# Kernel optimization log

Measured on AMD Instinct MI355X. Metric: run time of the kernel, lower is better.

The kernel has to match this reference:

```python
import jax, jax.numpy as jnp
import numpy as np

TOP_K = 2
AUX_COEF = 1e-3

def setup_inputs() -> dict:
    key = jax.random.key(0)
    ks = jax.random.split(key, 5)
    B, S, H, I, E = 4, 2048, 1024, 2048, 8
    x = jax.random.normal(ks[0], (B, S, H), jnp.float32)
    gate_w = jax.random.normal(ks[1], (H, E), jnp.float32) * 0.02
    w_gate = jax.random.normal(ks[2], (E, H, I), jnp.float32) * 0.02
    w_up = jax.random.normal(ks[3], (E, H, I), jnp.float32) * 0.02
    w_down = jax.random.normal(ks[4], (E, I, H), jnp.float32) * 0.02
    return {"x": x, "gate_w": gate_w, "w_gate": w_gate, "w_up": w_up, "w_down": w_down}


def reference(x, gate_w, w_gate, w_up, w_down):
    B, S, H = x.shape
    E = gate_w.shape[1]
    xf = x.reshape(-1, H)              # [N, H]
    N = xf.shape[0]

    # Router: softmax in fp32 (matches F.softmax(..., dtype=torch.float32))
    logits = xf @ gate_w               # [N, E]
    rw = jax.nn.softmax(logits.astype(jnp.float32), axis=-1).astype(x.dtype)
    top_w, top_i = jax.lax.top_k(rw, TOP_K)            # [N, K]
    top_w = top_w / top_w.sum(axis=-1, keepdims=True)  # renormalize

    # Combine weights: comb[t, e] = sum_k top_w[t,k] * (top_i[t,k]==e)
    comb = jnp.zeros((N, E), x.dtype).at[jnp.arange(N)[:, None], top_i].add(top_w)

    # SwiGLU FFN computed densely per expert, masked/combined by router weights
    h_gate = jax.nn.silu(jnp.einsum('th,ehi->eti', xf, w_gate))   # [E, N, I]
    h_up = jnp.einsum('th,ehi->eti', xf, w_up)                    # [E, N, I]
    expert_out = jnp.einsum('eti,eih->eth', h_gate * h_up, w_down)  # [E, N, H]
    y = jnp.einsum('eth,te->th', expert_out, comb).reshape(B, S, H)

    # Load-balancing aux loss
    sel_w = jnp.take_along_axis(rw, top_i, axis=1)   # router weight of chosen experts [N, K]
    load = jnp.zeros((E,), rw.dtype).at[top_i.reshape(-1)].add(sel_w.reshape(-1))
    P_expert = load / N
    counts = jnp.zeros((E,), jnp.float32).at[top_i.reshape(-1)].add(1.0)
    P_token_expert = counts / (N * TOP_K)
    aux_loss = (P_expert * P_token_expert).sum() * E * AUX_COEF
    return y, aux_loss
```

## Files before the change

kernel.cpp:

```cpp
#include <hip/hip_runtime.h>

#define N_TOK 8192
#define H_DIM 1024
#define I_DIM 2048
#define N_EXP 8
#define TOPK  2
#define CAP   17408
#define MT_MAX 136

#define OFF_TOPK_I 0u
#define OFF_TOPK_W 65536u
#define OFF_COUNTS 131072u
#define OFF_LOAD   131104u
#define OFF_CURSOR 131136u
#define OFF_PO     131168u
#define OFF_TILE_E 131232u
#define OFF_BTOK   131840u
#define OFF_BW     201472u
#define CTRL_BYTES 271104u
#define OFF_TSLOT  271104u
#define OFF_WGT  1048576u
#define OFF_WUT  (OFF_WGT + 33554432u)
#define OFF_WDT  (OFF_WUT + 33554432u)
#define OFF_HB   (OFF_WDT + 33554432u)
#define OFF_XB   (OFF_HB + 71303168u)

typedef __attribute__((ext_vector_type(8))) short bf16x8;
typedef __attribute__((ext_vector_type(8))) unsigned short u16x8;
typedef __attribute__((ext_vector_type(4))) unsigned short u16x4;
typedef __attribute__((ext_vector_type(4))) float f32x4;

__device__ __forceinline__ unsigned short f2bf(float f) {
  union { float f; unsigned int u; } v; v.f = f;
  unsigned int r = (v.u + 0x7FFFu + ((v.u >> 16) & 1u)) >> 16;
  return (unsigned short)r;
}
__device__ __forceinline__ float bf2f(unsigned short u) {
  union { unsigned int u; float f; } v; v.u = ((unsigned int)u) << 16;
  return v.f;
}
__device__ __forceinline__ u16x8 pack8(float4 a, float4 b) {
  u16x8 r;
  r[0] = f2bf(a.x); r[1] = f2bf(a.y); r[2] = f2bf(a.z); r[3] = f2bf(a.w);
  r[4] = f2bf(b.x); r[5] = f2bf(b.y); r[6] = f2bf(b.z); r[7] = f2bf(b.w);
  return r;
}
__device__ __forceinline__ f32x4 mfma32(bf16x8 a, bf16x8 b, f32x4 c) {
  return __builtin_amdgcn_mfma_f32_16x16x32_bf16(a, b, c, 0, 0, 0);
}
__device__ __forceinline__ void gll16(const void* g, void* l) {
  __builtin_amdgcn_global_load_lds(
      (const __attribute__((address_space(1))) unsigned int*)g,
      (__attribute__((address_space(3))) unsigned int*)l, 16, 0, 0);
}

__global__ __launch_bounds__(256) void k_xcast(const float* __restrict__ x,
                                               unsigned short* __restrict__ xb)
{
  int idx = blockIdx.x * 256 + threadIdx.x;
  const float4* s = (const float4*)x + (size_t)idx * 2;
  float4 a = s[0], b = s[1];
  *(u16x8*)&xb[(size_t)idx * 8] = pack8(a, b);
}

__global__ __launch_bounds__(256) void k_transpose(
    const float* __restrict__ wg, const float* __restrict__ wu, const float* __restrict__ wd,
    unsigned short* __restrict__ wgT, unsigned short* __restrict__ wuT,
    unsigned short* __restrict__ wdT)
{
  __shared__ unsigned short lds[64][65];
  int bid = blockIdx.x;
  int m = bid / 4096; int rem = bid % 4096;
  const float* src; unsigned short* dst; int R, C;
  if (m == 0)      { src = wg; dst = wgT; R = 1024; C = 2048; }
  else if (m == 1) { src = wu; dst = wuT; R = 1024; C = 2048; }
  else             { src = wd; dst = wdT; R = 2048; C = 1024; }
  int e = rem / 512; int trem = rem % 512;
  int tcc = C / 64;
  int r0 = (trem / tcc) * 64, c0 = (trem % tcc) * 64;
  size_t ebase = (size_t)e * R * C;
  dst += ebase;
  int tid = threadIdx.x;
  int lr = tid >> 3;
  int lc = (tid & 7) * 8;
#pragma unroll
  for (int p = 0; p < 2; ++p) {
    int row = p * 32 + lr;
    size_t off = ebase + (size_t)(r0 + row) * C + c0 + lc;
    float4 q0 = *(const float4*)&src[off];
    float4 q1 = *(const float4*)&src[off + 4];
    unsigned short tmp[8]; *(u16x8*)tmp = pack8(q0, q1);
#pragma unroll
    for (int j = 0; j < 8; ++j) lds[row][lc + j] = tmp[j];
  }
  __syncthreads();
#pragma unroll
  for (int p = 0; p < 2; ++p) {
    int drow = p * 32 + lr;
    unsigned short tmp[8];
#pragma unroll
    for (int j = 0; j < 8; ++j) tmp[j] = lds[lc + j][drow];
    *(u16x8*)&dst[(size_t)(c0 + drow) * R + r0 + lc] = *(const u16x8*)tmp;
  }
}

__global__ __launch_bounds__(256) void k_router(
    const float* __restrict__ x, const float* __restrict__ gw,
    int* __restrict__ topk_i, float* __restrict__ topk_w)
{
  int wave = threadIdx.x >> 6, lane = threadIdx.x & 63;
  int t = blockIdx.x * 4 + wave;
  const float* xr = x + (size_t)t * H_DIM;
  float acc[8];
#pragma unroll
  for (int e = 0; e < 8; ++e) acc[e] = 0.f;
#pragma unroll
  for (int it = 0; it < H_DIM / 64; ++it) {
    int h = it * 64 + lane;
    float xv = xr[h];
    float4 g0 = *(const float4*)&gw[h * 8];
    float4 g1 = *(const float4*)&gw[h * 8 + 4];
    acc[0] += xv * g0.x; acc[1] += xv * g0.y; acc[2] += xv * g0.z; acc[3] += xv * g0.w;
    acc[4] += xv * g1.x; acc[5] += xv * g1.y; acc[6] += xv * g1.z; acc[7] += xv * g1.w;
  }
#pragma unroll
  for (int off = 32; off > 0; off >>= 1) {
#pragma unroll
    for (int e = 0; e < 8; ++e) acc[e] += __shfl_xor(acc[e], off);
  }
  if (lane == 0) {
    float m = acc[0];
#pragma unroll
    for (int e = 1; e < 8; ++e) m = fmaxf(m, acc[e]);
    float p[8], s = 0.f;
#pragma unroll
    for (int e = 0; e < 8; ++e) { p[e] = __expf(acc[e] - m); s += p[e]; }
    float inv = 1.f / s;
#pragma unroll
    for (int e = 0; e < 8; ++e) p[e] *= inv;
    int i1 = 0;
#pragma unroll
    for (int e = 1; e < 8; ++e) if (p[e] > p[i1]) i1 = e;
    int i2 = (i1 == 0) ? 1 : 0;
#pragma unroll
    for (int e = 0; e < 8; ++e) if (e != i1 && p[e] > p[i2]) i2 = e;
    topk_i[t * 2]     = i1; topk_i[t * 2 + 1] = i2;
    topk_w[t * 2]     = p[i1]; topk_w[t * 2 + 1] = p[i2];
  }
}

__global__ __launch_bounds__(256) void k_hist(
    const int* __restrict__ topk_i, const float* __restrict__ topk_w,
    int* __restrict__ counts, float* __restrict__ loadw)
{
  __shared__ int c[8]; __shared__ float l[8];
  int tid = threadIdx.x;
  if (tid < 8) { c[tid] = 0; l[tid] = 0.f; }
  __syncthreads();
  int base = blockIdx.x * 1024 + tid * 4;
#pragma unroll
  for (int j = 0; j < 4; ++j) {
    int e = topk_i[base + j];
    float w = topk_w[base + j];
    atomicAdd(&c[e], 1);
    atomicAdd(&l[e], w);
  }
  __syncthreads();
  if (tid < 8) { atomicAdd(&counts[tid], c[tid]); atomicAdd(&loadw[tid], l[tid]); }
}

__global__ __launch_bounds__(256) void k_offsets(
    const int* __restrict__ counts, const float* __restrict__ loadw,
    int* __restrict__ po, int* __restrict__ tile_e, float* __restrict__ out)
{
  __shared__ int spo[9];
  if (threadIdx.x == 0) {
    int a = 0;
    for (int e = 0; e < 8; ++e) { spo[e] = a; po[e] = a; a += (counts[e] + 127) & ~127; }
    spo[8] = a; po[8] = a;
    float s = 0.f;
    for (int e = 0; e < 8; ++e) s += loadw[e] * (float)counts[e];
    out[(size_t)N_TOK * H_DIM] =
        s * ((float)N_EXP * 1e-3f) / ((float)N_TOK * (float)N_TOK * (float)TOPK);
  }
  __syncthreads();
  int mt = threadIdx.x;
  if (mt < MT_MAX) {
    int te = -1, beg = mt * 128;
    if (beg < spo[8]) {
      for (int e = 0; e < 8; ++e) if (beg >= spo[e] && beg < spo[e + 1]) te = e;
    }
    tile_e[mt] = te;
  }
}

__global__ __launch_bounds__(256) void k_bucket(
    const int* __restrict__ topk_i, const float* __restrict__ topk_w,
    const int* __restrict__ po, int* __restrict__ cursor,
    int* __restrict__ btok, float* __restrict__ bw, int* __restrict__ tslot)
{
  __shared__ int c[8];
  __shared__ int basee[8];
  int tid = threadIdx.x;
  if (tid < 8) c[tid] = 0;
  __syncthreads();
  int base = blockIdx.x * 1024 + tid * 4;
  int e4[4], r4[4]; float w4[4];
#pragma unroll
  for (int j = 0; j < 4; ++j) {
    int idx = base + j;
    int e = topk_i[idx];
    e4[j] = e;
    r4[j] = atomicAdd(&c[e], 1);
    int t = idx >> 1;
    float p0 = topk_w[t * 2], p1 = topk_w[t * 2 + 1];
    w4[j] = topk_w[idx] / (p0 + p1);
  }
  __syncthreads();
  if (tid < 8) basee[tid] = po[tid] + atomicAdd(&cursor[tid], c[tid]);
  __syncthreads();
#pragma unroll
  for (int j = 0; j < 4; ++j) {
    int idx = base + j;
    int slot = basee[e4[j]] + r4[j];
    btok[slot] = idx >> 1;
    bw[slot] = w4[j];
    tslot[idx] = slot;
  }
}

__global__ __launch_bounds__(256, 2) void k_gemm1(
    const unsigned short* __restrict__ xb,
    const unsigned short* __restrict__ wgT, const unsigned short* __restrict__ wuT,
    const int* __restrict__ btok, const int* __restrict__ tile_e,
    unsigned short* __restrict__ hbuf)
{
  int mt = blockIdx.y, nt = blockIdx.x;
  int e = tile_e[mt];
  if (e < 0) return;
  __shared__ unsigned short As[128 * 32];
  __shared__ unsigned short Bg[128 * 32];
  __shared__ unsigned short Bu[128 * 32];
  int tid = threadIdx.x;
  int wave = tid >> 6, lane = tid & 63;
  int wm = wave >> 1, wn = wave & 1;
  int quad = lane >> 4, l16 = lane & 15;

  int srow = lane >> 2;
  int sko  = (lane & 3) * 8;
  int ar0 = wave * 16 + srow;
  int ar1 = 64 + wave * 16 + srow;
  int t0 = btok[mt * 128 + ar0];
  int t1 = btok[mt * 128 + ar1];
  const unsigned short* ga0 = xb + (size_t)t0 * H_DIM + sko;
  const unsigned short* ga1 = xb + (size_t)t1 * H_DIM + sko;
  const unsigned short* bgb = wgT + ((size_t)e * I_DIM + nt * 128) * H_DIM;
  const unsigned short* bub = wuT + ((size_t)e * I_DIM + nt * 128) * H_DIM;
  const unsigned short* gg0 = bgb + (size_t)ar0 * H_DIM + sko;
  const unsigned short* gg1 = bgb + (size_t)ar1 * H_DIM + sko;
  const unsigned short* gu0 = bub + (size_t)ar0 * H_DIM + sko;
  const unsigned short* gu1 = bub + (size_t)ar1 * H_DIM + sko;
  unsigned lb0 = (unsigned)(wave * 16) * 32;
  unsigned lb1 = (unsigned)(64 + wave * 16) * 32;

  f32x4 accG[4][4], accU[4][4];
  f32x4 z = {0.f, 0.f, 0.f, 0.f};
#pragma unroll
  for (int i = 0; i < 4; ++i)
#pragma unroll
    for (int j = 0; j < 4; ++j) { accG[i][j] = z; accU[i][j] = z; }

  for (int k0 = 0; k0 < H_DIM; k0 += 32) {
    gll16(ga0 + k0, &As[lb0]);
    gll16(ga1 + k0, &As[lb1]);
    gll16(gg0 + k0, &Bg[lb0]);
    gll16(gg1 + k0, &Bg[lb1]);
    gll16(gu0 + k0, &Bu[lb0]);
    gll16(gu1 + k0, &Bu[lb1]);
    __syncthreads();
    bf16x8 af[4];
#pragma unroll
    for (int i = 0; i < 4; ++i)
      af[i] = *(const bf16x8*)&As[(wm * 64 + i * 16 + l16) * 32 + quad * 8];
#pragma unroll
    for (int j = 0; j < 4; ++j) {
      bf16x8 vg = *(const bf16x8*)&Bg[(wn * 64 + j * 16 + l16) * 32 + quad * 8];
      bf16x8 vu = *(const bf16x8*)&Bu[(wn * 64 + j * 16 + l16) * 32 + quad * 8];
#pragma unroll
      for (int i = 0; i < 4; ++i) {
        accG[i][j] = mfma32(af[i], vg, accG[i][j]);
        accU[i][j] = mfma32(af[i], vu, accU[i][j]);
      }
    }
    __syncthreads();
  }
#pragma unroll
  for (int i = 0; i < 4; ++i) {
#pragma unroll
    for (int r = 0; r < 4; ++r) {
      int row = mt * 128 + wm * 64 + i * 16 + quad * 4 + r;
      size_t base = (size_t)row * I_DIM + nt * 128 + wn * 64 + l16;
#pragma unroll
      for (int j = 0; j < 4; ++j) {
        float g = accG[i][j][r], u = accU[i][j][r];
        float sg = g / (1.f + __expf(-g));
        hbuf[base + j * 16] = f2bf(sg * u);
      }
    }
  }
}

__global__ __launch_bounds__(256, 2) void k_gemm2(
    const unsigned short* __restrict__ hbuf, const unsigned short* __restrict__ wdT,
    const int* __restrict__ tile_e, unsigned short* __restrict__ obuf)
{
  int mt = blockIdx.y, nt = blockIdx.x;
  int e = tile_e[mt];
  if (e < 0) return;
  __shared__ unsigned short As[128 * 32];
  __shared__ unsigned short Bs[128 * 32];
  int tid = threadIdx.x;
  int wave = tid >> 6, lane = tid & 63;
  int wm = wave >> 1, wn = wave & 1;
  int quad = lane >> 4, l16 = lane & 15;

  int srow = lane >> 2;
  int sko  = (lane & 3) * 8;
  int ar0 = wave * 16 + srow;
  int ar1 = 64 + wave * 16 + srow;
  const unsigned short* ga0 = hbuf + (size_t)(mt * 128 + ar0) * I_DIM + sko;
  const unsigned short* ga1 = hbuf + (size_t)(mt * 128 + ar1) * I_DIM + sko;
  const unsigned short* bb = wdT + ((size_t)e * H_DIM + nt * 128) * I_DIM;
  const unsigned short* gb0 = bb + (size_t)ar0 * I_DIM + sko;
  const unsigned short* gb1 = bb + (size_t)ar1 * I_DIM + sko;
  unsigned lb0 = (unsigned)(wave * 16) * 32;
  unsigned lb1 = (unsigned)(64 + wave * 16) * 32;

  f32x4 acc[4][4];
  f32x4 z = {0.f, 0.f, 0.f, 0.f};
#pragma unroll
  for (int i = 0; i < 4; ++i)
#pragma unroll
    for (int j = 0; j < 4; ++j) acc[i][j] = z;

  for (int k0 = 0; k0 < I_DIM; k0 += 32) {
    gll16(ga0 + k0, &As[lb0]);
    gll16(ga1 + k0, &As[lb1]);
    gll16(gb0 + k0, &Bs[lb0]);
    gll16(gb1 + k0, &Bs[lb1]);
    __syncthreads();
    bf16x8 af[4];
#pragma unroll
    for (int i = 0; i < 4; ++i)
      af[i] = *(const bf16x8*)&As[(wm * 64 + i * 16 + l16) * 32 + quad * 8];
#pragma unroll
    for (int j = 0; j < 4; ++j) {
      bf16x8 vb = *(const bf16x8*)&Bs[(wn * 64 + j * 16 + l16) * 32 + quad * 8];
#pragma unroll
      for (int i = 0; i < 4; ++i) acc[i][j] = mfma32(af[i], vb, acc[i][j]);
    }
    __syncthreads();
  }
#pragma unroll
  for (int i = 0; i < 4; ++i) {
#pragma unroll
    for (int r = 0; r < 4; ++r) {
      int s = mt * 128 + wm * 64 + i * 16 + quad * 4 + r;
      size_t base = (size_t)s * H_DIM + nt * 128 + wn * 64 + l16;
#pragma unroll
      for (int j = 0; j < 4; ++j)
        obuf[base + j * 16] = f2bf(acc[i][j][r]);
    }
  }
}

__global__ __launch_bounds__(256) void k_final(
    const unsigned short* __restrict__ obuf, const int* __restrict__ tslot,
    const float* __restrict__ bw, float* __restrict__ y)
{
  int t = blockIdx.x;
  int s0 = tslot[t * 2], s1 = tslot[t * 2 + 1];
  float w0 = bw[s0], w1 = bw[s1];
  int c = threadIdx.x * 4;
  u16x4 o0 = *(const u16x4*)&obuf[(size_t)s0 * H_DIM + c];
  u16x4 o1 = *(const u16x4*)&obuf[(size_t)s1 * H_DIM + c];
  float4 r;
  r.x = w0 * bf2f(o0[0]) + w1 * bf2f(o1[0]);
  r.y = w0 * bf2f(o0[1]) + w1 * bf2f(o1[1]);
  r.z = w0 * bf2f(o0[2]) + w1 * bf2f(o1[2]);
  r.w = w0 * bf2f(o0[3]) + w1 * bf2f(o1[3]);
  *(float4*)&y[(size_t)t * H_DIM + c] = r;
}

extern "C" void kernel_launch(void* const* d_in, const int* in_sizes, int n_in,
                              void* d_out, int out_size, void* d_ws, size_t ws_size,
                              hipStream_t stream)
{
  (void)in_sizes; (void)n_in; (void)out_size; (void)ws_size;
  const float* x  = (const float*)d_in[0];
  const float* gw = (const float*)d_in[1];
  const float* wg = (const float*)d_in[2];
  const float* wu = (const float*)d_in[3];
  const float* wd = (const float*)d_in[4];
  char* ws = (char*)d_ws;

  int*   topk_i = (int*)  (ws + OFF_TOPK_I);
  float* topk_w = (float*)(ws + OFF_TOPK_W);
  int*   counts = (int*)  (ws + OFF_COUNTS);
  float* loadw  = (float*)(ws + OFF_LOAD);
  int*   cursor = (int*)  (ws + OFF_CURSOR);
  int*   po     = (int*)  (ws + OFF_PO);
  int*   tile_e = (int*)  (ws + OFF_TILE_E);
  int*   btok   = (int*)  (ws + OFF_BTOK);
  float* bw     = (float*)(ws + OFF_BW);
  int*   tslot  = (int*)  (ws + OFF_TSLOT);
  unsigned short* wgT  = (unsigned short*)(ws + OFF_WGT);
  unsigned short* wuT  = (unsigned short*)(ws + OFF_WUT);
  unsigned short* wdT  = (unsigned short*)(ws + OFF_WDT);
  unsigned short* hbuf = (unsigned short*)(ws + OFF_HB);
  unsigned short* xb   = (unsigned short*)(ws + OFF_XB);
  unsigned short* obuf = (unsigned short*)(ws + OFF_WGT);
  float* yout = (float*)d_out;

  (void)hipMemsetAsync(ws, 0, CTRL_BYTES, stream);
  k_xcast<<<(N_TOK * H_DIM) / 2048, 256, 0, stream>>>(x, xb);
  k_transpose<<<12288, 256, 0, stream>>>(wg, wu, wd, wgT, wuT, wdT);
  k_router<<<N_TOK / 4, 256, 0, stream>>>(x, gw, topk_i, topk_w);
  k_hist<<<16, 256, 0, stream>>>(topk_i, topk_w, counts, loadw);
  k_offsets<<<1, 256, 0, stream>>>(counts, loadw, po, tile_e, (float*)d_out);
  k_bucket<<<16, 256, 0, stream>>>(topk_i, topk_w, po, cursor, btok, bw, tslot);
  k_gemm1<<<dim3(I_DIM / 128, MT_MAX), 256, 0, stream>>>(xb, wgT, wuT, btok, tile_e, hbuf);
  k_gemm2<<<dim3(H_DIM / 128, MT_MAX), 256, 0, stream>>>(hbuf, wdT, tile_e, obuf);
  k_final<<<N_TOK, 256, 0, stream>>>(obuf, tslot, bw, yout);
}
```

Before: 575.9 us.

## Double-buffer and swizzle grouped GEMMs, fuse cast and histogram into router

Both grouped GEMM kernels switch to double-buffered LDS. The next k-slice is fetched with global_load_lds while MFMAs run on the current one, leaving one barrier per iteration instead of two. LDS columns get an XOR swizzle to cut bank conflicts, and MFMA sections run at raised wave priority. The grid is reordered so consecutive blocks walk M tiles for the same weight N tile, which should improve L2 reuse of expert weights. The separate x cast and histogram kernels are folded into the router, which writes bf16 x and does global atomics directly; this saves launches but uses scalar 2-byte stores and global atomics in their place.

```diff
diff --git a/kernel.cpp b/kernel.cpp
--- a/kernel.cpp
+++ b/kernel.cpp
@@ -30,6 +30,11 @@
 typedef __attribute__((ext_vector_type(4))) unsigned short u16x4;
 typedef __attribute__((ext_vector_type(4))) float f32x4;
 
+#define BAR() __builtin_amdgcn_s_barrier()
+#define PRIO1() __builtin_amdgcn_s_setprio(1)
+#define PRIO0() __builtin_amdgcn_s_setprio(0)
+#define WAITV0() asm volatile("s_waitcnt vmcnt(0)" ::: "memory")
+
 __device__ __forceinline__ unsigned short f2bf(float f) {
   union { float f; unsigned int u; } v; v.f = f;
   unsigned int r = (v.u + 0x7FFFu + ((v.u >> 16) & 1u)) >> 16;
@@ -52,15 +57,6 @@
   __builtin_amdgcn_global_load_lds(
       (const __attribute__((address_space(1))) unsigned int*)g,
       (__attribute__((address_space(3))) unsigned int*)l, 16, 0, 0);
-}
-
-__global__ __launch_bounds__(256) void k_xcast(const float* __restrict__ x,
-                                               unsigned short* __restrict__ xb)
-{
-  int idx = blockIdx.x * 256 + threadIdx.x;
-  const float4* s = (const float4*)x + (size_t)idx * 2;
-  float4 a = s[0], b = s[1];
-  *(u16x8*)&xb[(size_t)idx * 8] = pack8(a, b);
 }
 
 __global__ __launch_bounds__(256) void k_transpose(
@@ -106,7 +102,9 @@
 
 __global__ __launch_bounds__(256) void k_router(
     const float* __restrict__ x, const float* __restrict__ gw,
-    int* __restrict__ topk_i, float* __restrict__ topk_w)
+    unsigned short* __restrict__ xb,
+    int* __restrict__ topk_i, float* __restrict__ topk_w,
+    int* __restrict__ counts, float* __restrict__ loadw)
 {
   int wave = threadIdx.x >> 6, lane = threadIdx.x & 63;
   int t = blockIdx.x * 4 + wave;
@@ -118,6 +116,7 @@
   for (int it = 0; it < H_DIM / 64; ++it) {
     int h = it * 64 + lane;
     float xv = xr[h];
+    xb[(size_t)t * H_DIM + h] = f2bf(xv);
     float4 g0 = *(const float4*)&gw[h * 8];
     float4 g1 = *(const float4*)&gw[h * 8 + 4];
     acc[0] += xv * g0.x; acc[1] += xv * g0.y; acc[2] += xv * g0.z; acc[3] += xv * g0.w;
@@ -146,27 +145,9 @@
     for (int e = 0; e < 8; ++e) if (e != i1 && p[e] > p[i2]) i2 = e;
     topk_i[t * 2]     = i1; topk_i[t * 2 + 1] = i2;
     topk_w[t * 2]     = p[i1]; topk_w[t * 2 + 1] = p[i2];
-  }
-}
-
-__global__ __launch_bounds__(256) void k_hist(
-    const int* __restrict__ topk_i, const float* __restrict__ topk_w,
-    int* __restrict__ counts, float* __restrict__ loadw)
-{
-  __shared__ int c[8]; __shared__ float l[8];
-  int tid = threadIdx.x;
-  if (tid < 8) { c[tid] = 0; l[tid] = 0.f; }
-  __syncthreads();
-  int base = blockIdx.x * 1024 + tid * 4;
-#pragma unroll
-  for (int j = 0; j < 4; ++j) {
-    int e = topk_i[base + j];
-    float w = topk_w[base + j];
-    atomicAdd(&c[e], 1);
-    atomicAdd(&l[e], w);
-  }
-  __syncthreads();
-  if (tid < 8) { atomicAdd(&counts[tid], c[tid]); atomicAdd(&loadw[tid], l[tid]); }
+    atomicAdd(&counts[i1], 1); atomicAdd(&counts[i2], 1);
+    atomicAdd(&loadw[i1], p[i1]); atomicAdd(&loadw[i2], p[i2]);
+  }
 }
 
 __global__ __launch_bounds__(256) void k_offsets(
@@ -235,33 +216,30 @@
     const int* __restrict__ btok, const int* __restrict__ tile_e,
     unsigned short* __restrict__ hbuf)
 {
-  int mt = blockIdx.y, nt = blockIdx.x;
+  int mt = blockIdx.x, nt = blockIdx.y;
   int e = tile_e[mt];
   if (e < 0) return;
-  __shared__ unsigned short As[128 * 32];
-  __shared__ unsigned short Bg[128 * 32];
-  __shared__ unsigned short Bu[128 * 32];
+  __shared__ unsigned short lds[24576];
   int tid = threadIdx.x;
   int wave = tid >> 6, lane = tid & 63;
   int wm = wave >> 1, wn = wave & 1;
   int quad = lane >> 4, l16 = lane & 15;
 
-  int srow = lane >> 2;
-  int sko  = (lane & 3) * 8;
-  int ar0 = wave * 16 + srow;
-  int ar1 = 64 + wave * 16 + srow;
-  int t0 = btok[mt * 128 + ar0];
-  int t1 = btok[mt * 128 + ar1];
-  const unsigned short* ga0 = xb + (size_t)t0 * H_DIM + sko;
-  const unsigned short* ga1 = xb + (size_t)t1 * H_DIM + sko;
-  const unsigned short* bgb = wgT + ((size_t)e * I_DIM + nt * 128) * H_DIM;
-  const unsigned short* bub = wuT + ((size_t)e * I_DIM + nt * 128) * H_DIM;
-  const unsigned short* gg0 = bgb + (size_t)ar0 * H_DIM + sko;
-  const unsigned short* gg1 = bgb + (size_t)ar1 * H_DIM + sko;
-  const unsigned short* gu0 = bub + (size_t)ar0 * H_DIM + sko;
-  const unsigned short* gu1 = bub + (size_t)ar1 * H_DIM + sko;
-  unsigned lb0 = (unsigned)(wave * 16) * 32;
-  unsigned lb1 = (unsigned)(64 + wave * 16) * 32;
+  int rl = lane >> 2;
+  int cw = lane & 3;
+  int scol = (cw ^ ((rl >> 1) & 3)) * 8;
+  const unsigned short* sA[2]; const unsigned short* sBg[2]; const unsigned short* sBu[2];
+  unsigned dA[2];
+#pragma unroll
+  for (int c = 0; c < 2; ++c) {
+    int row = wave * 32 + c * 16 + rl;
+    int tok = btok[mt * 128 + row];
+    sA[c]  = xb + (size_t)tok * H_DIM + scol;
+    sBg[c] = wgT + ((size_t)e * I_DIM + nt * 128 + row) * H_DIM + scol;
+    sBu[c] = wuT + ((size_t)e * I_DIM + nt * 128 + row) * H_DIM + scol;
+    dA[c]  = (unsigned)(wave * 32 + c * 16) * 32;
+  }
+  int fsw = (l16 >> 1) & 3;
 
   f32x4 accG[4][4], accU[4][4];
   f32x4 z = {0.f, 0.f, 0.f, 0.f};
@@ -270,71 +248,91 @@
 #pragma unroll
     for (int j = 0; j < 4; ++j) { accG[i][j] = z; accU[i][j] = z; }
 
-  for (int k0 = 0; k0 < H_DIM; k0 += 32) {
-    gll16(ga0 + k0, &As[lb0]);
-    gll16(ga1 + k0, &As[lb1]);
-    gll16(gg0 + k0, &Bg[lb0]);
-    gll16(gg1 + k0, &Bg[lb1]);
-    gll16(gu0 + k0, &Bu[lb0]);
-    gll16(gu1 + k0, &Bu[lb1]);
-    __syncthreads();
-    bf16x8 af[4];
-#pragma unroll
-    for (int i = 0; i < 4; ++i)
-      af[i] = *(const bf16x8*)&As[(wm * 64 + i * 16 + l16) * 32 + quad * 8];
-#pragma unroll
-    for (int j = 0; j < 4; ++j) {
-      bf16x8 vg = *(const bf16x8*)&Bg[(wn * 64 + j * 16 + l16) * 32 + quad * 8];
-      bf16x8 vu = *(const bf16x8*)&Bu[(wn * 64 + j * 16 + l16) * 32 + quad * 8];
-#pragma unroll
-      for (int i = 0; i < 4; ++i) {
-        accG[i][j] = mfma32(af[i], vg, accG[i][j]);
-        accU[i][j] = mfma32(af[i], vu, accU[i][j]);
+#pragma unroll
+  for (int c = 0; c < 2; ++c) {
+    gll16(sA[c],  &lds[dA[c]]);
+    gll16(sBg[c], &lds[4096u + dA[c]]);
+    gll16(sBu[c], &lds[8192u + dA[c]]);
+  }
+  WAITV0();
+  BAR();
+
+  for (int t = 0; t < 32; ++t) {
+    unsigned bo  = (t & 1) ? 12288u : 0u;
+    unsigned bo1 = 12288u - bo;
+    bf16x8 a[4], g[4], u[4];
+#pragma unroll
+    for (int m = 0; m < 4; ++m)
+      a[m] = *(const bf16x8*)&lds[bo + (unsigned)(wm * 64 + m * 16 + l16) * 32 + ((quad ^ fsw) * 8)];
+#pragma unroll
+    for (int nf = 0; nf < 4; ++nf) {
+      unsigned co = (unsigned)(wn * 64 + nf * 16 + l16) * 32 + ((quad ^ fsw) * 8);
+      g[nf] = *(const bf16x8*)&lds[bo + 4096u + co];
+      u[nf] = *(const bf16x8*)&lds[bo + 8192u + co];
+    }
+    if (t < 31) {
+      int kel = (t + 1) * 32;
+#pragma unroll
+      for (int c = 0; c < 2; ++c) {
+        gll16(sA[c] + kel,  &lds[bo1 + dA[c]]);
+        gll16(sBg[c] + kel, &lds[bo1 + 4096u + dA[c]]);
+        gll16(sBu[c] + kel, &lds[bo1 + 8192u + dA[c]]);
       }
     }
-    __syncthreads();
-  }
-#pragma unroll
-  for (int i = 0; i < 4; ++i) {
+    PRIO1();
+#pragma unroll
+    for (int nf = 0; nf < 4; ++nf)
+#pragma unroll
+      for (int m = 0; m < 4; ++m) accG[m][nf] = mfma32(a[m], g[nf], accG[m][nf]);
+#pragma unroll
+    for (int nf = 0; nf < 4; ++nf)
+#pragma unroll
+      for (int m = 0; m < 4; ++m) accU[m][nf] = mfma32(a[m], u[nf], accU[m][nf]);
+    PRIO0();
+    WAITV0();
+    BAR();
+  }
+#pragma unroll
+  for (int m = 0; m < 4; ++m)
 #pragma unroll
     for (int r = 0; r < 4; ++r) {
-      int row = mt * 128 + wm * 64 + i * 16 + quad * 4 + r;
+      int row = mt * 128 + wm * 64 + m * 16 + quad * 4 + r;
       size_t base = (size_t)row * I_DIM + nt * 128 + wn * 64 + l16;
 #pragma unroll
-      for (int j = 0; j < 4; ++j) {
-        float g = accG[i][j][r], u = accU[i][j][r];
-        float sg = g / (1.f + __expf(-g));
-        hbuf[base + j * 16] = f2bf(sg * u);
+      for (int nf = 0; nf < 4; ++nf) {
+        float gv = accG[m][nf][r], uv = accU[m][nf][r];
+        float sg = gv / (1.f + __expf(-gv));
+        hbuf[base + nf * 16] = f2bf(sg * uv);
       }
     }
-  }
-}
-
-__global__ __launch_bounds__(256, 2) void k_gemm2(
+}
+
+__global__ __launch_bounds__(256, 3) void k_gemm2(
     const unsigned short* __restrict__ hbuf, const unsigned short* __restrict__ wdT,
     const int* __restrict__ tile_e, unsigned short* __restrict__ obuf)
 {
-  int mt = blockIdx.y, nt = blockIdx.x;
+  int mt = blockIdx.x, nt = blockIdx.y;
   int e = tile_e[mt];
   if (e < 0) return;
-  __shared__ unsigned short As[128 * 32];
-  __shared__ unsigned short Bs[128 * 32];
+  __shared__ unsigned short lds[16384];
   int tid = threadIdx.x;
   int wave = tid >> 6, lane = tid & 63;
   int wm = wave >> 1, wn = wave & 1;
   int quad = lane >> 4, l16 = lane & 15;
 
-  int srow = lane >> 2;
-  int sko  = (lane & 3) * 8;
-  int ar0 = wave * 16 + srow;
-  int ar1 = 64 + wave * 16 + srow;
-  const unsigned short* ga0 = hbuf + (size_t)(mt * 128 + ar0) * I_DIM + sko;
-  const unsigned short* ga1 = hbuf + (size_t)(mt * 128 + ar1) * I_DIM + sko;
-  const unsigned short* bb = wdT + ((size_t)e * H_DIM + nt * 128) * I_DIM;
-  const unsigned short* gb0 = bb + (size_t)ar0 * I_DIM + sko;
-  const unsigned short* gb1 = bb + (size_t)ar1 * I_DIM + sko;
-  unsigned lb0 = (unsigned)(wave * 16) * 32;
-  unsigned lb1 = (unsigned)(64 + wave * 16) * 32;
+  int rl = lane >> 2;
+  int cw = lane & 3;
+  int scol = (cw ^ ((rl >> 1) & 3)) * 8;
+  const unsigned short* sA[2]; const unsigned short* sB[2];
+  unsigned dA[2];
+#pragma unroll
+  for (int c = 0; c < 2; ++c) {
+    int row = wave * 32 + c * 16 + rl;
+    sA[c] = hbuf + (size_t)(mt * 128 + row) * I_DIM + scol;
+    sB[c] = wdT + ((size_t)e * H_DIM + nt * 128 + row) * I_DIM + scol;
+    dA[c] = (unsigned)(wave * 32 + c * 16) * 32;
+  }
+  int fsw = (l16 >> 1) & 3;
 
   f32x4 acc[4][4];
   f32x4 z = {0.f, 0.f, 0.f, 0.f};
@@ -343,35 +341,51 @@
 #pragma unroll
     for (int j = 0; j < 4; ++j) acc[i][j] = z;
 
-  for (int k0 = 0; k0 < I_DIM; k0 += 32) {
-    gll16(ga0 + k0, &As[lb0]);
-    gll16(ga1 + k0, &As[lb1]);
-    gll16(gb0 + k0, &Bs[lb0]);
-    gll16(gb1 + k0, &Bs[lb1]);
-    __syncthreads();
-    bf16x8 af[4];
-#pragma unroll
-    for (int i = 0; i < 4; ++i)
-      af[i] = *(const bf16x8*)&As[(wm * 64 + i * 16 + l16) * 32 + quad * 8];
-#pragma unroll
-    for (int j = 0; j < 4; ++j) {
-      bf16x8 vb = *(const bf16x8*)&Bs[(wn * 64 + j * 16 + l16) * 32 + quad * 8];
-#pragma unroll
-      for (int i = 0; i < 4; ++i) acc[i][j] = mfma32(af[i], vb, acc[i][j]);
-    }
-    __syncthreads();
-  }
-#pragma unroll
-  for (int i = 0; i < 4; ++i) {
+#pragma unroll
+  for (int c = 0; c < 2; ++c) {
+    gll16(sA[c], &lds[dA[c]]);
+    gll16(sB[c], &lds[4096u + dA[c]]);
+  }
+  WAITV0();
+  BAR();
+
+  for (int t = 0; t < 64; ++t) {
+    unsigned bo  = (t & 1) ? 8192u : 0u;
+    unsigned bo1 = 8192u - bo;
+    bf16x8 a[4], b[4];
+#pragma unroll
+    for (int m = 0; m < 4; ++m)
+      a[m] = *(const bf16x8*)&lds[bo + (unsigned)(wm * 64 + m * 16 + l16) * 32 + ((quad ^ fsw) * 8)];
+#pragma unroll
+    for (int nf = 0; nf < 4; ++nf)
+      b[nf] = *(const bf16x8*)&lds[bo + 4096u + (unsigned)(wn * 64 + nf * 16 + l16) * 32 + ((quad ^ fsw) * 8)];
+    if (t < 63) {
+      int kel = (t + 1) * 32;
+#pragma unroll
+      for (int c = 0; c < 2; ++c) {
+        gll16(sA[c] + kel, &lds[bo1 + dA[c]]);
+        gll16(sB[c] + kel, &lds[bo1 + 4096u + dA[c]]);
+      }
+    }
+    PRIO1();
+#pragma unroll
+    for (int nf = 0; nf < 4; ++nf)
+#pragma unroll
+      for (int m = 0; m < 4; ++m) acc[m][nf] = mfma32(a[m], b[nf], acc[m][nf]);
+    PRIO0();
+    WAITV0();
+    BAR();
+  }
+#pragma unroll
+  for (int m = 0; m < 4; ++m)
 #pragma unroll
     for (int r = 0; r < 4; ++r) {
-      int s = mt * 128 + wm * 64 + i * 16 + quad * 4 + r;
+      int s = mt * 128 + wm * 64 + m * 16 + quad * 4 + r;
       size_t base = (size_t)s * H_DIM + nt * 128 + wn * 64 + l16;
 #pragma unroll
-      for (int j = 0; j < 4; ++j)
-        obuf[base + j * 16] = f2bf(acc[i][j][r]);
-    }
-  }
+      for (int nf = 0; nf < 4; ++nf)
+        obuf[base + nf * 16] = f2bf(acc[m][nf][r]);
+    }
 }
 
 __global__ __launch_bounds__(256) void k_final(
@@ -423,13 +437,11 @@
   float* yout = (float*)d_out;
 
   (void)hipMemsetAsync(ws, 0, CTRL_BYTES, stream);
-  k_xcast<<<(N_TOK * H_DIM) / 2048, 256, 0, stream>>>(x, xb);
+  k_router<<<N_TOK / 4, 256, 0, stream>>>(x, gw, xb, topk_i, topk_w, counts, loadw);
   k_transpose<<<12288, 256, 0, stream>>>(wg, wu, wd, wgT, wuT, wdT);
-  k_router<<<N_TOK / 4, 256, 0, stream>>>(x, gw, topk_i, topk_w);
-  k_hist<<<16, 256, 0, stream>>>(topk_i, topk_w, counts, loadw);
   k_offsets<<<1, 256, 0, stream>>>(counts, loadw, po, tile_e, (float*)d_out);
   k_bucket<<<16, 256, 0, stream>>>(topk_i, topk_w, po, cursor, btok, bw, tslot);
-  k_gemm1<<<dim3(I_DIM / 128, MT_MAX), 256, 0, stream>>>(xb, wgT, wuT, btok, tile_e, hbuf);
-  k_gemm2<<<dim3(H_DIM / 128, MT_MAX), 256, 0, stream>>>(hbuf, wdT, tile_e, obuf);
+  k_gemm1<<<dim3(MT_MAX, I_DIM / 128), 256, 0, stream>>>(xb, wgT, wuT, btok, tile_e, hbuf);
+  k_gemm2<<<dim3(MT_MAX, H_DIM / 128), 256, 0, stream>>>(hbuf, wdT, tile_e, obuf);
   k_final<<<N_TOK, 256, 0, stream>>>(obuf, tslot, bw, yout);
 }
```

Result: slower. 939.2 us (+63.1%).
